# Performance work log

Hardware: AMD Instinct MI355X
Metric: run time of the kernel (lower is better)

Reference implementation:

```python
import jax, jax.numpy as jnp
import numpy as np

B, S, DIM, H, G, DH = 1, 2048, 2048, 16, 2, 128
L, D, LP, NSEL, W = 32, 16, 32, 16, 256   # compress len, stride, select block, top-k blocks, window
REP = H // G


def setup_inputs() -> dict:
    key = jax.random.key(0)
    ks = jax.random.split(key, 8)
    x = jax.random.normal(ks[0], (B, S, DIM), jnp.float32)
    inv = 1.0 / (10000.0 ** (jnp.arange(0, DH, 2, dtype=jnp.float32) / DH))
    ang = jnp.outer(jnp.arange(S, dtype=jnp.float32), inv)   # [S, DH//2]
    freqs_cos, freqs_sin = jnp.cos(ang), jnp.sin(ang)
    std = 0.02
    wq = jax.random.normal(ks[1], (DIM, H * DH), jnp.float32) * std
    wk = jax.random.normal(ks[2], (DIM, G * DH), jnp.float32) * std
    wv = jax.random.normal(ks[3], (DIM, G * DH), jnp.float32) * std
    wo = jax.random.normal(ks[4], (H * DH, DIM), jnp.float32) * std
    w_g = jax.random.normal(ks[5], (DH, 3), jnp.float32) * std
    return dict(x=x, freqs_cos=freqs_cos, freqs_sin=freqs_sin,
                wq=wq, wk=wk, wv=wv, wo=wo, w_g=w_g, start_pos=0)


def _rope(t, cos, sin):
    # t: [B,S,heads,DH]; complex pairs are consecutive elements (view_as_complex semantics)
    x0, x1 = t[..., 0::2], t[..., 1::2]
    c, s = cos[None, :, None, :], sin[None, :, None, :]
    return jnp.stack([x0 * c - x1 * s, x0 * s + x1 * c], axis=-1).reshape(t.shape)


def _nsa_forward(x, freqs_cos, freqs_sin, wq, wk, wv, wo, w_g):
    scale = DH ** -0.5
    q = (x @ wq).reshape(B, S, H, DH)
    k = (x @ wk).reshape(B, S, G, DH)
    v = (x @ wv).reshape(B, S, G, DH)
    q = _rope(q, freqs_cos, freqs_sin).reshape(B, S, G, REP, DH)
    k = _rope(k, freqs_cos, freqs_sin)

    tpos = jnp.arange(S)
    NEG = jnp.float32(-1e30)

    # ---- branch 1: compressed-block attention ----
    J = (S - L) // D + 1
    starts = jnp.arange(J) * D
    blk_idx = starts[:, None] + jnp.arange(L)[None, :]            # [J, L]
    k_cmp = k[:, blk_idx].mean(axis=2)                            # [B,J,G,DH]
    v_cmp = v[:, blk_idx].mean(axis=2)
    s_cmp = jnp.einsum('bsgrd,bjgd->bsgrj', q, k_cmp) * scale
    valid = (starts[None, :] + L - 1) <= tpos[:, None]            # [S, J]
    p_cmp = jax.nn.softmax(jnp.where(valid[None, :, None, None, :], s_cmp, NEG), axis=-1)
    p_cmp = jnp.where(valid.any(-1)[None, :, None, None, None], p_cmp, 0.0)
    o_cmp = jnp.einsum('bsgrj,bjgd->bsgrd', p_cmp, v_cmp)

    # ---- branch 2: top-n selected-block attention ----
    NB = S // LP
    sel_start = jnp.arange(NB) * LP
    # overlap of cmp block [j*D, j*D+L) with selection block [m*LP, m*LP+LP)
    ov = (starts[:, None] < sel_start[None, :] + LP) & (starts[:, None] + L > sel_start[None, :])
    imp = jnp.einsum('bsgrj,jm->bsgm', p_cmp, ov.astype(jnp.float32))   # sum over heads in group
    blk_causal = sel_start[None, :] <= tpos[:, None]                    # [S, NB]
    imp = jnp.where(blk_causal[None, :, None, :], imp, -jnp.inf)
    cur_blk = tpos // LP
    force = jax.nn.one_hot(cur_blk, NB) + jax.nn.one_hot(jnp.zeros_like(cur_blk), NB)
    imp = imp + force[None, :, None, :] * 1e9                           # always keep init + current block
    _, top_idx = jax.lax.top_k(imp, NSEL)                               # [B,S,G,NSEL]
    blk_mask = jax.nn.one_hot(top_idx, NB).sum(axis=-2) > 0             # [B,S,G,NB]
    tok_sel = jnp.repeat(blk_mask, LP, axis=-1)                         # [B,S,G,S]
    causal = tpos[:, None] >= tpos[None, :]                             # [S,S]

    s_full = jnp.einsum('bsgrd,btgd->bsgrt', q, k) * scale              # [B,S,G,R,S]
    m_sel = tok_sel[:, :, :, None, :] & causal[None, :, None, None, :]
    p_sel = jax.nn.softmax(jnp.where(m_sel, s_full, NEG), axis=-1)
    o_sel = jnp.einsum('bsgrt,btgd->bsgrd', p_sel, v)

    # ---- branch 3: sliding-window attention ----
    m_sw = causal & (tpos[None, :] > tpos[:, None] - W)
    p_sw = jax.nn.softmax(jnp.where(m_sw[None, :, None, None, :], s_full, NEG), axis=-1)
    o_sw = jnp.einsum('bsgrt,btgd->bsgrd', p_sw, v)

    # ---- learned gated combination ----
    g = jax.nn.sigmoid(jnp.einsum('bsgrd,de->bsgre', q, w_g))
    out = g[..., 0:1] * o_cmp + g[..., 1:2] * o_sel + g[..., 2:3] * o_sw
    return out.reshape(B, S, H * DH) @ wo


def reference(x, freqs_cos, freqs_sin, wq, wk, wv, wo, w_g, start_pos):
    return _nsa_forward(x, freqs_cos, freqs_sin, wq, wk, wv, wo, w_g)
```

## Files before the change

kernel.cpp:

```cpp
#include <hip/hip_runtime.h>
#include <cstddef>
#include <cstdint>
#include <math.h>

#define kS    2048
#define kDim  2048
#define kH    16
#define kG    2
#define kDH   128
#define kRep  8
#define kL    32
#define kDstr 16
#define kLP   32
#define kNSel 16
#define kW    256
#define kJ    127
#define kNB   64
#define kScale 0.08838834764831845f
#define kQT   4
#define kQF   8
#define kLDQ  2560

#define kKP   136
#define kVP   40

typedef __attribute__((ext_vector_type(4))) float f32x4;
typedef __attribute__((ext_vector_type(8))) __bf16 bf16x8;
typedef __attribute__((ext_vector_type(4))) __bf16 bf16x4;

__device__ __forceinline__ unsigned short f2bf(float f) {
  unsigned u = __float_as_uint(f);
  u += 0x7fff + ((u >> 16) & 1);
  return (unsigned short)(u >> 16);
}

#define GLDS16(src, dst)                                                     \
  __builtin_amdgcn_global_load_lds(                                          \
      (const __attribute__((address_space(1))) unsigned int*)(src),          \
      (__attribute__((address_space(3))) unsigned int*)(dst), 16, 0, 0)

__global__ void cast_bf16_kernel(const float* __restrict__ in,
                                 unsigned short* __restrict__ out, int n4) {
  int i = blockIdx.x * blockDim.x + threadIdx.x;
  if (i >= n4) return;
  float4 v = reinterpret_cast<const float4*>(in)[i];
  ushort4 o;
  o.x = f2bf(v.x); o.y = f2bf(v.y); o.z = f2bf(v.z); o.w = f2bf(v.w);
  reinterpret_cast<ushort4*>(out)[i] = o;
}

__global__ void cast_rows_kernel(const float* __restrict__ in, int ldin,
                                 unsigned short* __restrict__ out, int ldout,
                                 int row4, int total4) {
  int i = blockIdx.x * blockDim.x + threadIdx.x;
  if (i >= total4) return;
  int r = i / row4;
  int c4 = i - r * row4;
  float4 v = *reinterpret_cast<const float4*>(in + (size_t)r * ldin + c4 * 4);
  ushort4 o;
  o.x = f2bf(v.x); o.y = f2bf(v.y); o.z = f2bf(v.z); o.w = f2bf(v.w);
  *reinterpret_cast<ushort4*>(out + (size_t)r * ldout + c4 * 4) = o;
}

__global__ __launch_bounds__(256) void transpose_cast_kernel(
    const float* __restrict__ in, int ldin, unsigned short* __restrict__ out,
    int rows, int cols) {
  __shared__ float tile[32][33];
  const int bx = blockIdx.x * 32;
  const int by = blockIdx.y * 32;
  const int tx = threadIdx.x & 31;
  const int ty = threadIdx.x >> 5;
#pragma unroll
  for (int i = 0; i < 32; i += 8)
    tile[ty + i][tx] = in[(size_t)(by + ty + i) * ldin + bx + tx];
  __syncthreads();
#pragma unroll
  for (int i = 0; i < 32; i += 8)
    out[(size_t)(bx + ty + i) * rows + by + tx] = f2bf(tile[tx][ty + i]);
}

__global__ __launch_bounds__(512) void gemm_bf16_kernel(
    const unsigned short* __restrict__ A,
    const unsigned short* __restrict__ Bt,
    float* __restrict__ C, int M, int N, int ldc, int K) {
  __shared__ __align__(16) unsigned short As[128 * 32];
  __shared__ __align__(16) unsigned short Bs[128 * 32];
  const int t = threadIdx.x;
  const int lane = t & 63;
  const int wid = t >> 6;
  const int wr = wid >> 2;
  const int wc = wid & 3;
  const int lhi = lane >> 4, llo = lane & 15;
  const size_t row0 = (size_t)blockIdx.y * 128;
  const size_t col0 = (size_t)blockIdx.x * 128;

  f32x4 acc[4][2];
#pragma unroll
  for (int m = 0; m < 4; ++m)
#pragma unroll
    for (int n = 0; n < 2; ++n) acc[m][n] = f32x4{0.f, 0.f, 0.f, 0.f};

  const int e0 = t * 8;
  const int r0 = e0 >> 5, kk0 = e0 & 31;

  for (int k0 = 0; k0 < K; k0 += 32) {
    GLDS16(A + (row0 + r0) * (size_t)K + k0 + kk0, As + e0);
    GLDS16(Bt + (col0 + r0) * (size_t)K + k0 + kk0, Bs + e0);
    __syncthreads();
    bf16x8 af[4], bfr[2];
#pragma unroll
    for (int m = 0; m < 4; ++m)
      af[m] = *reinterpret_cast<const bf16x8*>(&As[(wr * 64 + m * 16 + llo) * 32 + lhi * 8]);
#pragma unroll
    for (int n = 0; n < 2; ++n)
      bfr[n] = *reinterpret_cast<const bf16x8*>(&Bs[(wc * 32 + n * 16 + llo) * 32 + lhi * 8]);
#pragma unroll
    for (int m = 0; m < 4; ++m)
#pragma unroll
      for (int n = 0; n < 2; ++n)
        acc[m][n] = __builtin_amdgcn_mfma_f32_16x16x32_bf16(af[m], bfr[n], acc[m][n], 0, 0, 0);
    __syncthreads();
  }
#pragma unroll
  for (int m = 0; m < 4; ++m)
#pragma unroll
    for (int n = 0; n < 2; ++n)
#pragma unroll
      for (int j = 0; j < 4; ++j) {
        size_t r = row0 + wr * 64 + m * 16 + lhi * 4 + j;
        size_t c = col0 + wc * 32 + n * 16 + llo;
        C[r * (size_t)ldc + c] = acc[m][n][j];
      }
}

__global__ void rope_kernel(float* __restrict__ tb, int ld,
                            const float* __restrict__ fc,
                            const float* __restrict__ fsn, int nheads, int total) {
  int idx = blockIdx.x * blockDim.x + threadIdx.x;
  if (idx >= total) return;
  int i = idx & 63;
  int h = (idx >> 6) % nheads;
  int s = idx / (64 * nheads);
  float c = fc[s * 64 + i];
  float sn = fsn[s * 64 + i];
  float* p = tb + (size_t)s * ld + h * kDH + 2 * i;
  float x0 = p[0], x1 = p[1];
  p[0] = x0 * c - x1 * sn;
  p[1] = x0 * sn + x1 * c;
}

__global__ void pool_kernel(const float* __restrict__ qkv,
                            float* __restrict__ kcT,
                            unsigned short* __restrict__ vcT) {
  int idx = blockIdx.x * blockDim.x + threadIdx.x;
  if (idx >= 128 * kG * kDH) return;
  int d = idx & 127;
  int g = (idx >> 7) & 1;
  int j = idx >> 8;
  float sk = 0.f, sv = 0.f;
  if (j < kJ) {
    for (int l = 0; l < kL; ++l) {
      size_t row = (size_t)(j * kDstr + l) * kLDQ;
      sk += qkv[row + kDim + g * kDH + d];
      sv += qkv[row + kDim + kG * kDH + g * kDH + d];
    }
    sk *= (1.f / 32.f);
    sv *= (1.f / 32.f);
  }
  size_t o = ((size_t)(g * 128 + d)) * 128 + j;
  kcT[o] = sk;
  vcT[o] = f2bf(sv);
}

__global__ __launch_bounds__(256) void cmp_attn_kernel(
    const float* __restrict__ qkv, const float* __restrict__ kcT,
    const unsigned short* __restrict__ vcT,
    const float* __restrict__ wg,
    float* __restrict__ oc, float* __restrict__ gates,
    unsigned long long* __restrict__ selmask) {
  __shared__ float qst[128][36];
  __shared__ float pT [128][36];
  __shared__ __align__(16) char ubuf[32 * 132 * 4];
  float (*kvt)[132] = reinterpret_cast<float(*)[132]>(ubuf);
  unsigned short (*pTb)[136] = reinterpret_cast<unsigned short(*)[136]>(ubuf);

  const int b = blockIdx.x;
  const int g = b & 1;
  const int s0 = (b >> 1) * kQT;
  const int t = threadIdx.x;
  const int ty = t >> 5;
  const int tx = t & 31;

  {
    int row = t & 31;
    int dl = (t >> 5) * 16;
    const float* src = qkv + (size_t)(s0 + (row >> 3)) * kLDQ +
                       (g * kRep + (row & 7)) * kDH + dl;
#pragma unroll
    for (int i = 0; i < 4; ++i) {
      float4 v = *reinterpret_cast<const float4*>(src + i * 4);
      qst[dl + i * 4 + 0][row] = v.x;
      qst[dl + i * 4 + 1][row] = v.y;
      qst[dl + i * 4 + 2][row] = v.z;
      qst[dl + i * 4 + 3][row] = v.w;
    }
  }
  __syncthreads();

  float S[4][4];
#pragma unroll
  for (int rr = 0; rr < 4; ++rr)
#pragma unroll
    for (int jj = 0; jj < 4; ++jj) S[rr][jj] = 0.f;

  for (int dt = 0; dt < 4; ++dt) {
    {
      const float* base = kcT + (size_t)(g * 128 + dt * 32) * 128;
#pragma unroll
      for (int i = 0; i < 4; ++i) {
        int s = t + i * 256;
        int dd = s >> 5;
        int j4 = s & 31;
        *reinterpret_cast<float4*>(&kvt[dd][j4 * 4]) =
            *reinterpret_cast<const float4*>(base + dd * 128 + j4 * 4);
      }
    }
    __syncthreads();
#pragma unroll
    for (int kk = 0; kk < 32; ++kk) {
      float4 a = *reinterpret_cast<const float4*>(&qst[dt * 32 + kk][ty * 4]);
      float4 bb = *reinterpret_cast<const float4*>(&kvt[kk][tx * 4]);
      float av[4] = {a.x, a.y, a.z, a.w};
      float bv[4] = {bb.x, bb.y, bb.z, bb.w};
#pragma unroll
      for (int rr = 0; rr < 4; ++rr)
#pragma unroll
        for (int jj = 0; jj < 4; ++jj)
          S[rr][jj] = fmaf(av[rr], bv[jj], S[rr][jj]);
    }
    __syncthreads();
  }

#pragma unroll
  for (int rr = 0; rr < 4; ++rr) {
    int row = ty * 4 + rr;
    int s = s0 + (row >> 3);
    int jmax = (s >= kL - 1) ? ((s - (kL - 1)) >> 4) : -1;
#pragma unroll
    for (int jj = 0; jj < 4; ++jj) {
      int j = tx * 4 + jj;
      pT[j][row] = (j <= jmax && j < kJ) ? S[rr][jj] * kScale : -1e30f;
    }
  }
  __syncthreads();

  {
    int row = t >> 3;
    int l = t & 7;
    int s = s0 + (row >> 3);
    if (s < kL - 1) {
#pragma unroll
      for (int i = 0; i < 16; ++i) pT[l + i * 8][row] = 0.f;
    } else {
      float vals[16];
      float mx = -INFINITY;
#pragma unroll
      for (int i = 0; i < 16; ++i) {
        vals[i] = pT[l + i * 8][row];
        mx = fmaxf(mx, vals[i]);
      }
      mx = fmaxf(mx, __shfl_xor(mx, 1));
      mx = fmaxf(mx, __shfl_xor(mx, 2));
      mx = fmaxf(mx, __shfl_xor(mx, 4));
      float sm = 0.f;
#pragma unroll
      for (int i = 0; i < 16; ++i) {
        vals[i] = __expf(vals[i] - mx);
        sm += vals[i];
      }
      sm += __shfl_xor(sm, 1);
      sm += __shfl_xor(sm, 2);
      sm += __shfl_xor(sm, 4);
      float inv = 1.f / sm;
#pragma unroll
      for (int i = 0; i < 16; ++i) pT[l + i * 8][row] = vals[i] * inv;
    }
  }
  __syncthreads();

  {
    int row = t >> 3;
    int l = t & 7;
#pragma unroll
    for (int i = 0; i < 16; ++i)
      pTb[row][l + i * 8] = f2bf(pT[l + i * 8][row]);
  }
  {
    int qq = t >> 6;
    int m = t & 63;
    int s = s0 + qq;
    int mcur = s >> 5;
    float im;
    if (m > mcur) {
      im = -INFINITY;
    } else {
      im = 0.f;
#pragma unroll
      for (int r = 0; r < 8; ++r) {
        int row = qq * 8 + r;
        float sp = (2 * m - 1 >= 0) ? pT[2 * m - 1][row] : 0.f;
        sp += pT[2 * m][row];
        if (2 * m + 1 < kJ) sp += pT[2 * m + 1][row];
        im += sp;
      }
      if (m == 0) im += 1e9f;
      if (m == mcur) im += 1e9f;
    }
    bool taken = false;
    unsigned long long mask = 0ull;
    for (int it = 0; it < kNSel; ++it) {
      float cv = taken ? -INFINITY : im;
      int ci = taken ? 64 : m;
#pragma unroll
      for (int off = 1; off < 64; off <<= 1) {
        float ov = __shfl_xor(cv, off);
        int oi = __shfl_xor(ci, off);
        if (ov > cv || (ov == cv && oi < ci)) { cv = ov; ci = oi; }
      }
      mask |= 1ull << ci;
      if (m == ci) taken = true;
    }
    if (m == 0) selmask[(size_t)s * 2 + g] = mask;
  }
  if (t < 192) {
    int task = t >> 1;
    int p = t & 1;
    int row = task / 3;
    int e = task - row * 3;
    int sQ = s0 + (row >> 3);
    int r = row & 7;
    const float* qr = qkv + (size_t)sQ * kLDQ + (g * kRep + r) * kDH + p * 64;
    float acc = 0.f;
#pragma unroll
    for (int i = 0; i < 16; ++i) {
      float4 v = *reinterpret_cast<const float4*>(qr + i * 4);
      int d = p * 64 + i * 4;
      acc = fmaf(v.x, wg[d * 3 + e], acc);
      acc = fmaf(v.y, wg[(d + 1) * 3 + e], acc);
      acc = fmaf(v.z, wg[(d + 2) * 3 + e], acc);
      acc = fmaf(v.w, wg[(d + 3) * 3 + e], acc);
    }
    acc += __shfl_xor(acc, 1);
    if (p == 0)
      gates[((size_t)(sQ * 2 + g) * kRep + r) * 3 + e] = 1.f / (1.f + __expf(-acc));
  }
  __syncthreads();

  {
    const int lane = t & 63;
    const int wv = t >> 6;
    const int lo = lane & 15, hi = lane >> 4;
    f32x4 acc[2][2];
#pragma unroll
    for (int rt = 0; rt < 2; ++rt)
#pragma unroll
      for (int dt2 = 0; dt2 < 2; ++dt2) acc[rt][dt2] = f32x4{0.f, 0.f, 0.f, 0.f};
#pragma unroll
    for (int ks = 0; ks < 4; ++ks) {
      bf16x8 pf[2], vf[2];
#pragma unroll
      for (int rt = 0; rt < 2; ++rt)
        pf[rt] = *reinterpret_cast<const bf16x8*>(&pTb[rt * 16 + lo][ks * 32 + hi * 8]);
#pragma unroll
      for (int dt2 = 0; dt2 < 2; ++dt2)
        vf[dt2] = *reinterpret_cast<const bf16x8*>(
            vcT + ((size_t)(g * 128 + wv * 32 + dt2 * 16 + lo)) * 128 + ks * 32 + hi * 8);
#pragma unroll
      for (int rt = 0; rt < 2; ++rt)
#pragma unroll
        for (int dt2 = 0; dt2 < 2; ++dt2)
          acc[rt][dt2] = __builtin_amdgcn_mfma_f32_16x16x32_bf16(vf[dt2], pf[rt], acc[rt][dt2], 0, 0, 0);
    }
#pragma unroll
    for (int rt = 0; rt < 2; ++rt) {
      int qrow = rt * 16 + lo;
      size_t base = ((size_t)(s0 + (qrow >> 3)) * kH + g * kRep + (qrow & 7)) * kDH;
#pragma unroll
      for (int dt2 = 0; dt2 < 2; ++dt2) {
        int d0 = wv * 32 + dt2 * 16 + hi * 4;
#pragma unroll
        for (int jj = 0; jj < 4; ++jj)
          oc[base + d0 + jj] = acc[rt][dt2][jj];
      }
    }
  }
}

template <int MODE>
__device__ __forceinline__ void attn_tile3(
    const unsigned short* __restrict__ Ksb, const unsigned short* __restrict__ VTb,
    const bf16x8 (&qf)[4], __bf16* Psw,
    int tb, unsigned selw, int wv, int lo, int hi, int s0,
    f32x4 (&O)[8], float& mst, float& lst) {
  f32x4 S0 = f32x4{0.f, 0.f, 0.f, 0.f};
  f32x4 S1 = f32x4{0.f, 0.f, 0.f, 0.f};
  __builtin_amdgcn_s_setprio(1);
#pragma unroll
  for (int ds = 0; ds < 4; ++ds) {
    bf16x8 a0 = *reinterpret_cast<const bf16x8*>(&Ksb[lo * kKP + ds * 32 + hi * 8]);
    bf16x8 a1 = *reinterpret_cast<const bf16x8*>(&Ksb[(16 + lo) * kKP + ds * 32 + hi * 8]);
    S0 = __builtin_amdgcn_mfma_f32_16x16x32_bf16(a0, qf[ds], S0, 0, 0, 0);
    S1 = __builtin_amdgcn_mfma_f32_16x16x32_bf16(a1, qf[ds], S1, 0, 0, 0);
  }
  __builtin_amdgcn_s_setprio(0);
  const int qloc = wv * 2 + (lo >> 3);
  const int s_row = s0 + qloc;
  const bool selq = (MODE == 1) || (((selw >> qloc) & 1u) != 0);
  float sv[2][4];
#pragma unroll
  for (int j = 0; j < 4; ++j) { sv[0][j] = S0[j]; sv[1][j] = S1[j]; }
#pragma unroll
  for (int tf = 0; tf < 2; ++tf)
#pragma unroll
    for (int j = 0; j < 4; ++j) {
      int tok = tb + tf * 16 + hi * 4 + j;
      bool ok = selq && (tok <= s_row) && (MODE == 0 || tok > s_row - kW);
      sv[tf][j] = ok ? sv[tf][j] * kScale : -1e30f;
    }
  float pm = sv[0][0];
#pragma unroll
  for (int tf = 0; tf < 2; ++tf)
#pragma unroll
    for (int j = 0; j < 4; ++j) pm = fmaxf(pm, sv[tf][j]);
  pm = fmaxf(pm, __shfl_xor(pm, 16));
  pm = fmaxf(pm, __shfl_xor(pm, 32));
  if (__any(pm > mst + 8.f)) {
    float mn = fmaxf(mst, pm);
    float f = __expf(mst - mn);
#pragma unroll
    for (int df = 0; df < 8; ++df)
#pragma unroll
      for (int j = 0; j < 4; ++j) O[df][j] *= f;
    lst *= f;
    mst = mn;
  }
  float lacc = 0.f;
#pragma unroll
  for (int tf = 0; tf < 2; ++tf) {
    bf16x4 pk;
#pragma unroll
    for (int j = 0; j < 4; ++j) {
      float e = __expf(sv[tf][j] - mst);
      lacc += e;
      pk[j] = (__bf16)e;
    }
    *reinterpret_cast<bf16x4*>(&Psw[lo * 40 + tf * 16 + hi * 4]) = pk;
  }
  lst += lacc;
  bf16x8 pfrag = *reinterpret_cast<const bf16x8*>(&Psw[lo * 40 + hi * 8]);
  __builtin_amdgcn_s_setprio(1);
#pragma unroll
  for (int df = 0; df < 8; ++df) {
    bf16x8 vf = *reinterpret_cast<const bf16x8*>(&VTb[(df * 16 + lo) * kVP + hi * 8]);
    O[df] = __builtin_amdgcn_mfma_f32_16x16x32_bf16(vf, pfrag, O[df], 0, 0, 0);
  }
  __builtin_amdgcn_s_setprio(0);
}

__global__ __launch_bounds__(256) void fused_attn_kernel(
    const unsigned short* __restrict__ qb, const unsigned short* __restrict__ kb,
    const unsigned short* __restrict__ vT, const float* __restrict__ ocp,
    const float* __restrict__ gts,
    const unsigned long long* __restrict__ selmask,
    unsigned short* __restrict__ preb) {
  __shared__ __align__(16) unsigned short Ks[2][32 * kKP];
  __shared__ __align__(16) unsigned short VTs[2][128 * kVP];
  __shared__ __align__(16) __bf16 Ps[4][16 * 40];
  __shared__ unsigned long long qm[kQF];
  __shared__ unsigned char selbits[kNB];
  __shared__ unsigned char blist[kNB];
  __shared__ int nsel_sh;

  const int g = blockIdx.x & 1;
  const int qt = blockIdx.x >> 1;
  const int s0 = qt * kQF;
  const int t = threadIdx.x;
  const int lane = t & 63;
  const int wv = t >> 6;
  const int lo = lane & 15, hi = lane >> 4;

  int kBase[3], vBase[3];
#pragma unroll
  for (int ii = 0; ii < 3; ++ii) {
    int s = t + ii * 256;
    int r = s / 17, c = s - r * 17;
    if (c > 15) c = 0;
    kBase[ii] = r * 256 + g * 128 + c * 8;
    int r2 = s / 5, c2 = s - r2 * 5;
    if (c2 > 3) c2 = 0;
    vBase[ii] = (g * 128 + r2) * 2048 + c2 * 8;
  }
  auto STAGE = [&](int tb, unsigned short* Ksb, unsigned short* VTb) {
#pragma unroll
    for (int ii = 0; ii < 3; ++ii) {
      if (ii < 2 || t < 32)
        GLDS16(kb + (size_t)tb * 256 + kBase[ii], Ksb + (t + ii * 256) * 8);
      if (ii < 2 || t < 128)
        GLDS16(vT + (size_t)vBase[ii] + tb, VTb + (t + ii * 256) * 8);
    }
  };

  const int qrow = wv * 16 + lo;
  const int s_q = s0 + (qrow >> 3);
  const int hd = qrow & 7;
  bf16x8 qf[4];
  {
    const unsigned short* src = qb + ((size_t)s_q * 16 + g * 8 + hd) * 128 + hi * 8;
#pragma unroll
    for (int ds = 0; ds < 4; ++ds)
      qf[ds] = *reinterpret_cast<const bf16x8*>(src + ds * 32);
  }
  if (t < kQF) {
    int sQ = s0 + t;
    unsigned long long mm = selmask[(size_t)sQ * 2 + g];
    mm &= ((2ull << (sQ >> 5)) - 1ull);
    qm[t] = mm;
  }
  __syncthreads();
  if (t < kNB) {
    unsigned b = 0;
    for (int ql = 0; ql < kQF; ++ql)
      b |= (unsigned)((qm[ql] >> t) & 1ull) << ql;
    selbits[t] = (unsigned char)b;
  }
  if (t == 0) {
    unsigned long long u = 0;
    for (int ql = 0; ql < kQF; ++ql) u |= qm[ql];
    int n = 0;
    for (int m = 0; m < kNB; ++m)
      if ((u >> m) & 1ull) blist[n++] = (unsigned char)m;
    nsel_sh = n;
  }
  __syncthreads();

  __bf16* Psw = &Ps[wv][0];

  f32x4 O1[8], O2[8];
#pragma unroll
  for (int df = 0; df < 8; ++df) O1[df] = f32x4{0.f, 0.f, 0.f, 0.f};
  float mst = -INFINITY, lst = 0.f;

  const int nsel = nsel_sh;
  int cur = 0;
  STAGE((int)blist[0] * 32, Ks[0], VTs[0]);
  __syncthreads();
  for (int i = 0; i < nsel; ++i) {
    if (i + 1 < nsel)
      STAGE((int)blist[i + 1] * 32, Ks[cur ^ 1], VTs[cur ^ 1]);
    int b = blist[i];
    attn_tile3<0>(Ks[cur], VTs[cur], qf, Psw, b * 32, selbits[b], wv, lo, hi, s0,
                  O1, mst, lst);
    __syncthreads();
    cur ^= 1;
  }
  const int hi_t = s0 >> 5;
  const int lo_t = (s0 > 255) ? ((s0 - 255) >> 5) : 0;
  STAGE(hi_t * 32, Ks[cur], VTs[cur]);
  float g0v, g2v;
  {
    const float* gp = gts + ((size_t)(s_q * 2 + g) * 8 + hd) * 3;
    g0v = gp[0];
    g2v = gp[2];
    float lt = lst;
    lt += __shfl_xor(lt, 16);
    lt += __shfl_xor(lt, 32);
    float f = gp[1] / lt;
#pragma unroll
    for (int df = 0; df < 8; ++df)
#pragma unroll
      for (int j = 0; j < 4; ++j) O1[df][j] *= f;
  }
  mst = -INFINITY;
  lst = 0.f;
#pragma unroll
  for (int df = 0; df < 8; ++df) O2[df] = f32x4{0.f, 0.f, 0.f, 0.f};
  __syncthreads();

  for (int tt = hi_t; tt >= lo_t; --tt) {
    if (tt - 1 >= lo_t)
      STAGE((tt - 1) * 32, Ks[cur ^ 1], VTs[cur ^ 1]);
    attn_tile3<1>(Ks[cur], VTs[cur], qf, Psw, tt * 32, 0u, wv, lo, hi, s0,
                  O2, mst, lst);
    __syncthreads();
    cur ^= 1;
  }

  {
    float lt = lst;
    lt += __shfl_xor(lt, 16);
    lt += __shfl_xor(lt, 32);
    float f2 = g2v / lt;
    size_t base = ((size_t)s_q * 16 + g * 8 + hd) * 128;
#pragma unroll
    for (int df = 0; df < 8; ++df) {
      int d0 = df * 16 + hi * 4;
      float4 ocv = *reinterpret_cast<const float4*>(&ocp[base + d0]);
      ushort4 w;
      w.x = f2bf(g0v * ocv.x + O1[df][0] + f2 * O2[df][0]);
      w.y = f2bf(g0v * ocv.y + O1[df][1] + f2 * O2[df][1]);
      w.z = f2bf(g0v * ocv.z + O1[df][2] + f2 * O2[df][2]);
      w.w = f2bf(g0v * ocv.w + O1[df][3] + f2 * O2[df][3]);
      *reinterpret_cast<ushort4*>(&preb[base + d0]) = w;
    }
  }
}

extern "C" void kernel_launch(void* const* d_in, const int* in_sizes, int n_in,
                              void* d_out, int out_size, void* d_ws, size_t ws_size,
                              hipStream_t stream) {
  (void)in_sizes; (void)n_in; (void)out_size; (void)ws_size;
  const float* x  = (const float*)d_in[0];
  const float* fc = (const float*)d_in[1];
  const float* fs = (const float*)d_in[2];
  const float* wq = (const float*)d_in[3];
  const float* wk = (const float*)d_in[4];
  const float* wv = (const float*)d_in[5];
  const float* wo = (const float*)d_in[6];
  const float* wg = (const float*)d_in[7];
  float* out = (float*)d_out;

  float* qkv  = (float*)d_ws;
  float* kcT  = qkv + (size_t)kS * kLDQ;
  float* oc   = kcT + 256 * 128;
  float* gts  = oc + kS * kH * kDH;
  unsigned long long* selmask = (unsigned long long*)(gts + kS * kG * kRep * 3);
  unsigned short* xb   = (unsigned short*)(selmask + kS * kG);
  unsigned short* wqT  = xb + kS * kDim;
  unsigned short* wkT  = wqT + (kH * kDH) * kDim;
  unsigned short* wvT  = wkT + (kG * kDH) * kDim;
  unsigned short* woT  = wvT + (kG * kDH) * kDim;
  unsigned short* preb = woT + kDim * (kH * kDH);
  unsigned short* kb   = preb + kS * kDim;
  unsigned short* vT   = kb + kS * kG * kDH;
  unsigned short* vcTb = vT + kS * kG * kDH;
  unsigned short* qbuf = xb;

  dim3 blk256(256);
  dim3 blk512(512);
  cast_bf16_kernel<<<kS * kDim / 4 / 256, blk256, 0, stream>>>(x, xb, kS * kDim / 4);
  transpose_cast_kernel<<<dim3((kH * kDH) / 32, kDim / 32), blk256, 0, stream>>>(wq, kH * kDH, wqT, kDim, kH * kDH);
  transpose_cast_kernel<<<dim3((kG * kDH) / 32, kDim / 32), blk256, 0, stream>>>(wk, kG * kDH, wkT, kDim, kG * kDH);
  transpose_cast_kernel<<<dim3((kG * kDH) / 32, kDim / 32), blk256, 0, stream>>>(wv, kG * kDH, wvT, kDim, kG * kDH);
  transpose_cast_kernel<<<dim3(kDim / 32, (kH * kDH) / 32), blk256, 0, stream>>>(wo, kDim, woT, kH * kDH, kDim);
  gemm_bf16_kernel<<<dim3(kLDQ / 128, kS / 128), blk512, 0, stream>>>(
      xb, wqT, qkv, kS, kLDQ, kLDQ, kDim);
  rope_kernel<<<8192, blk256, 0, stream>>>(qkv, kLDQ, fc, fs, kH, kS * kH * 64);
  rope_kernel<<<1024, blk256, 0, stream>>>(qkv + kDim, kLDQ, fc, fs, kG, kS * kG * 64);
  cast_rows_kernel<<<kS * kDim / 4 / 256, blk256, 0, stream>>>(
      qkv, kLDQ, qbuf, kDim, kDim / 4, kS * kDim / 4);
  cast_rows_kernel<<<kS * kG * kDH / 4 / 256, blk256, 0, stream>>>(
      qkv + kDim, kLDQ, kb, kG * kDH, kG * kDH / 4, kS * kG * kDH / 4);
  transpose_cast_kernel<<<dim3(kG * kDH / 32, kS / 32), blk256, 0, stream>>>(
      qkv + kDim + kG * kDH, kLDQ, vT, kS, kG * kDH);
  pool_kernel<<<128, blk256, 0, stream>>>(qkv, kcT, vcTb);
  cmp_attn_kernel<<<kS / kQT * kG, blk256, 0, stream>>>(qkv, kcT, vcTb, wg, oc, gts, selmask);
  fused_attn_kernel<<<kS / kQF * kG, blk256, 0, stream>>>(qbuf, kb, vT, oc, gts, selmask, preb);
  gemm_bf16_kernel<<<dim3(kDim / 128, kS / 128), blk512, 0, stream>>>(
      preb, woT, out, kS, kDim, kDim, kH * kDH);
}
```

Baseline: 274.2 us.

## Double query tile per attention block and fuse bf16 cast into RoPE

The fused attention kernel now processes 16 query positions per block with 512 threads (8 waves) instead of 8 with 256. Each staged K/V tile is therefore shared across twice as many query rows, which cuts global K/V traffic, and the selection bitmask widens to 16 bits. Separately, the RoPE kernel writes its bf16 copy directly, removing two cast_rows launches and the extra read of the fp32 q/k. Larger blocks halve the grid size and take the union of selected blocks over more queries, which may add masked work and reduce occupancy.

```diff
diff --git a/kernel.cpp b/kernel.cpp
--- a/kernel.cpp
+++ b/kernel.cpp
@@ -18,7 +18,7 @@
 #define kNB   64
 #define kScale 0.08838834764831845f
 #define kQT   4
-#define kQF   8
+#define kQF   16
 #define kLDQ  2560
 
 #define kKP   136
@@ -47,19 +47,6 @@
   ushort4 o;
   o.x = f2bf(v.x); o.y = f2bf(v.y); o.z = f2bf(v.z); o.w = f2bf(v.w);
   reinterpret_cast<ushort4*>(out)[i] = o;
-}
-
-__global__ void cast_rows_kernel(const float* __restrict__ in, int ldin,
-                                 unsigned short* __restrict__ out, int ldout,
-                                 int row4, int total4) {
-  int i = blockIdx.x * blockDim.x + threadIdx.x;
-  if (i >= total4) return;
-  int r = i / row4;
-  int c4 = i - r * row4;
-  float4 v = *reinterpret_cast<const float4*>(in + (size_t)r * ldin + c4 * 4);
-  ushort4 o;
-  o.x = f2bf(v.x); o.y = f2bf(v.y); o.z = f2bf(v.z); o.w = f2bf(v.w);
-  *reinterpret_cast<ushort4*>(out + (size_t)r * ldout + c4 * 4) = o;
 }
 
 __global__ __launch_bounds__(256) void transpose_cast_kernel(
@@ -135,7 +122,8 @@
 
 __global__ void rope_kernel(float* __restrict__ tb, int ld,
                             const float* __restrict__ fc,
-                            const float* __restrict__ fsn, int nheads, int total) {
+                            const float* __restrict__ fsn, int nheads, int total,
+                            unsigned short* __restrict__ outb, int ldout) {
   int idx = blockIdx.x * blockDim.x + threadIdx.x;
   if (idx >= total) return;
   int i = idx & 63;
@@ -145,8 +133,13 @@
   float sn = fsn[s * 64 + i];
   float* p = tb + (size_t)s * ld + h * kDH + 2 * i;
   float x0 = p[0], x1 = p[1];
-  p[0] = x0 * c - x1 * sn;
-  p[1] = x0 * sn + x1 * c;
+  float r0 = x0 * c - x1 * sn;
+  float r1 = x0 * sn + x1 * c;
+  p[0] = r0;
+  p[1] = r1;
+  unsigned short* o = outb + (size_t)s * ldout + h * kDH + 2 * i;
+  o[0] = f2bf(r0);
+  o[1] = f2bf(r1);
 }
 
 __global__ void pool_kernel(const float* __restrict__ qkv,
@@ -467,7 +460,7 @@
   __builtin_amdgcn_s_setprio(0);
 }
 
-__global__ __launch_bounds__(256) void fused_attn_kernel(
+__global__ __launch_bounds__(512) void fused_attn_kernel(
     const unsigned short* __restrict__ qb, const unsigned short* __restrict__ kb,
     const unsigned short* __restrict__ vT, const float* __restrict__ ocp,
     const float* __restrict__ gts,
@@ -475,9 +468,9 @@
     unsigned short* __restrict__ preb) {
   __shared__ __align__(16) unsigned short Ks[2][32 * kKP];
   __shared__ __align__(16) unsigned short VTs[2][128 * kVP];
-  __shared__ __align__(16) __bf16 Ps[4][16 * 40];
+  __shared__ __align__(16) __bf16 Ps[8][16 * 40];
   __shared__ unsigned long long qm[kQF];
-  __shared__ unsigned char selbits[kNB];
+  __shared__ unsigned short selbits[kNB];
   __shared__ unsigned char blist[kNB];
   __shared__ int nsel_sh;
 
@@ -489,10 +482,10 @@
   const int wv = t >> 6;
   const int lo = lane & 15, hi = lane >> 4;
 
-  int kBase[3], vBase[3];
-#pragma unroll
-  for (int ii = 0; ii < 3; ++ii) {
-    int s = t + ii * 256;
+  int kBase[2], vBase[2];
+#pragma unroll
+  for (int ii = 0; ii < 2; ++ii) {
+    int s = t + ii * 512;
     int r = s / 17, c = s - r * 17;
     if (c > 15) c = 0;
     kBase[ii] = r * 256 + g * 128 + c * 8;
@@ -501,13 +494,12 @@
     vBase[ii] = (g * 128 + r2) * 2048 + c2 * 8;
   }
   auto STAGE = [&](int tb, unsigned short* Ksb, unsigned short* VTb) {
-#pragma unroll
-    for (int ii = 0; ii < 3; ++ii) {
-      if (ii < 2 || t < 32)
-        GLDS16(kb + (size_t)tb * 256 + kBase[ii], Ksb + (t + ii * 256) * 8);
-      if (ii < 2 || t < 128)
-        GLDS16(vT + (size_t)vBase[ii] + tb, VTb + (t + ii * 256) * 8);
-    }
+    GLDS16(kb + (size_t)tb * 256 + kBase[0], Ksb + t * 8);
+    if (t < 32)
+      GLDS16(kb + (size_t)tb * 256 + kBase[1], Ksb + (t + 512) * 8);
+    GLDS16(vT + (size_t)vBase[0] + tb, VTb + t * 8);
+    if (t < 128)
+      GLDS16(vT + (size_t)vBase[1] + tb, VTb + (t + 512) * 8);
   };
 
   const int qrow = wv * 16 + lo;
@@ -531,7 +523,7 @@
     unsigned b = 0;
     for (int ql = 0; ql < kQF; ++ql)
       b |= (unsigned)((qm[ql] >> t) & 1ull) << ql;
-    selbits[t] = (unsigned char)b;
+    selbits[t] = (unsigned short)b;
   }
   if (t == 0) {
     unsigned long long u = 0;
@@ -654,17 +646,13 @@
   transpose_cast_kernel<<<dim3(kDim / 32, (kH * kDH) / 32), blk256, 0, stream>>>(wo, kDim, woT, kH * kDH, kDim);
   gemm_bf16_kernel<<<dim3(kLDQ / 128, kS / 128), blk512, 0, stream>>>(
       xb, wqT, qkv, kS, kLDQ, kLDQ, kDim);
-  rope_kernel<<<8192, blk256, 0, stream>>>(qkv, kLDQ, fc, fs, kH, kS * kH * 64);
-  rope_kernel<<<1024, blk256, 0, stream>>>(qkv + kDim, kLDQ, fc, fs, kG, kS * kG * 64);
-  cast_rows_kernel<<<kS * kDim / 4 / 256, blk256, 0, stream>>>(
-      qkv, kLDQ, qbuf, kDim, kDim / 4, kS * kDim / 4);
-  cast_rows_kernel<<<kS * kG * kDH / 4 / 256, blk256, 0, stream>>>(
-      qkv + kDim, kLDQ, kb, kG * kDH, kG * kDH / 4, kS * kG * kDH / 4);
+  rope_kernel<<<8192, blk256, 0, stream>>>(qkv, kLDQ, fc, fs, kH, kS * kH * 64, qbuf, kDim);
+  rope_kernel<<<1024, blk256, 0, stream>>>(qkv + kDim, kLDQ, fc, fs, kG, kS * kG * 64, kb, kG * kDH);
   transpose_cast_kernel<<<dim3(kG * kDH / 32, kS / 32), blk256, 0, stream>>>(
       qkv + kDim + kG * kDH, kLDQ, vT, kS, kG * kDH);
   pool_kernel<<<128, blk256, 0, stream>>>(qkv, kcT, vcTb);
   cmp_attn_kernel<<<kS / kQT * kG, blk256, 0, stream>>>(qkv, kcT, vcTb, wg, oc, gts, selmask);
-  fused_attn_kernel<<<kS / kQF * kG, blk256, 0, stream>>>(qbuf, kb, vT, oc, gts, selmask, preb);
+  fused_attn_kernel<<<kS / kQF * kG, blk512, 0, stream>>>(qbuf, kb, vT, oc, gts, selmask, preb);
   gemm_bf16_kernel<<<dim3(kDim / 128, kS / 128), blk512, 0, stream>>>(
       preb, woT, out, kS, kDim, kDim, kH * kDH);
 }
```

Result: no change. 279.0 us (+1.7%).
